# Optimization experiments

Hardware: AMD Instinct MI355X
Metric: run time of the kernel (lower is better)

The kernel has to match this reference:

```python
import jax, jax.numpy as jnp
import numpy as np
import math

NEG_BIG = -1e9

def setup_inputs() -> dict:
    key = jax.random.key(0)
    k1, k2, k3 = jax.random.split(key, 3)
    N, C, T = 16, 64, 2048
    qkv = jax.random.normal(k1, (N, 3 * C, T), dtype=jnp.float32)
    pos = jax.random.normal(k2, (N, C, T), dtype=jnp.float32)
    attn_mask = jax.random.randint(k3, (N, T, T), 0, 2) == 1  # bool mask, True = masked
    return {"qkv": qkv, "pos": pos, "attn_mask": attn_mask}

def reference(qkv, pos, attn_mask):
    ch = qkv.shape[1] // 3
    q, k, v = jnp.split(qkv, 3, axis=1)  # each [N, C, T]
    q = q + pos
    k = k + pos
    v = v + pos
    scale = 1.0 / math.sqrt(math.sqrt(ch))
    # [N, T, T] attention logits
    weight = jnp.einsum('bct,bcs->bts', q * scale, k * scale)
    weight = jnp.where(attn_mask, NEG_BIG, weight)
    weight = jax.nn.softmax(weight.astype(jnp.float32), axis=-1).astype(weight.dtype)
    return jnp.einsum('bts,bcs->bct', weight, v)
```

## Files before the change

kernel.cpp:

```cpp
#include <hip/hip_runtime.h>
#include <hip/hip_bf16.h>

typedef float f32x4 __attribute__((ext_vector_type(4)));
typedef short s16x8 __attribute__((ext_vector_type(8)));

#define L2E 1.44269504088896340736f

static __device__ __forceinline__ unsigned int bf16_rne(float f) {
    unsigned int u = __builtin_bit_cast(unsigned int, f);
    return (u + 0x7fffu + ((u >> 16) & 1u)) >> 16;
}
static __device__ __forceinline__ unsigned int pack_bf16x2(float lo, float hi) {
    return bf16_rne(lo) | (bf16_rne(hi) << 16);
}

__global__ __launch_bounds__(256) void qkv_prep(const float* __restrict__ qkv,
                                                const float* __restrict__ pos,
                                                unsigned short* __restrict__ qs,
                                                unsigned short* __restrict__ kt,
                                                unsigned short* __restrict__ vt)
{
    __shared__ unsigned short QtS[64][72];
    __shared__ unsigned short KtS[64][72];
    const int b    = blockIdx.y;
    const int t0   = blockIdx.x * 64;
    const int i    = threadIdx.x;
    const int crow = i >> 2;
    const int t16  = (i & 3) * 16;

    float pr[16];
    {
        const float* pp = pos + ((size_t)(b * 64 + crow)) * 2048 + t0 + t16;
        #pragma unroll
        for (int j = 0; j < 4; ++j) {
            float4 v = reinterpret_cast<const float4*>(pp)[j];
            pr[4*j+0] = v.x; pr[4*j+1] = v.y; pr[4*j+2] = v.z; pr[4*j+3] = v.w;
        }
    }
    const float* qp = qkv + ((size_t)(b * 192 + crow)) * 2048 + t0 + t16;
    {
        #pragma unroll
        for (int j = 0; j < 4; ++j) {
            float4 v = reinterpret_cast<const float4*>(qp)[j];
            QtS[t16 + 4*j + 0][crow] = (unsigned short)bf16_rne((v.x + pr[4*j+0]) * 0.125f);
            QtS[t16 + 4*j + 1][crow] = (unsigned short)bf16_rne((v.y + pr[4*j+1]) * 0.125f);
            QtS[t16 + 4*j + 2][crow] = (unsigned short)bf16_rne((v.z + pr[4*j+2]) * 0.125f);
            QtS[t16 + 4*j + 3][crow] = (unsigned short)bf16_rne((v.w + pr[4*j+3]) * 0.125f);
        }
    }
    {
        const float* kp = qp + (size_t)64 * 2048;
        #pragma unroll
        for (int j = 0; j < 4; ++j) {
            float4 v = reinterpret_cast<const float4*>(kp)[j];
            KtS[t16 + 4*j + 0][crow] = (unsigned short)bf16_rne(v.x + pr[4*j+0]);
            KtS[t16 + 4*j + 1][crow] = (unsigned short)bf16_rne(v.y + pr[4*j+1]);
            KtS[t16 + 4*j + 2][crow] = (unsigned short)bf16_rne(v.z + pr[4*j+2]);
            KtS[t16 + 4*j + 3][crow] = (unsigned short)bf16_rne(v.w + pr[4*j+3]);
        }
    }
    {
        const float* vp = qp + (size_t)128 * 2048;
        unsigned int vv[8];
        #pragma unroll
        for (int j = 0; j < 4; ++j) {
            float4 v = reinterpret_cast<const float4*>(vp)[j];
            vv[2*j+0] = pack_bf16x2(v.x + pr[4*j+0], v.y + pr[4*j+1]);
            vv[2*j+1] = pack_bf16x2(v.z + pr[4*j+2], v.w + pr[4*j+3]);
        }
        unsigned short* dst = vt + ((size_t)(b * 64 + crow)) * 2048 + t0 + t16;
        reinterpret_cast<uint4*>(dst)[0] = make_uint4(vv[0], vv[1], vv[2], vv[3]);
        reinterpret_cast<uint4*>(dst)[1] = make_uint4(vv[4], vv[5], vv[6], vv[7]);
    }
    __syncthreads();
    {
        const int trow = i >> 2;
        const int c16  = (i & 3) * 16;
        uint4 a0 = *reinterpret_cast<const uint4*>(&QtS[trow][c16]);
        uint4 a1 = *reinterpret_cast<const uint4*>(&QtS[trow][c16 + 8]);
        unsigned short* qd = qs + ((size_t)(b * 2048 + t0 + trow)) * 64 + c16;
        reinterpret_cast<uint4*>(qd)[0] = a0;
        reinterpret_cast<uint4*>(qd)[1] = a1;
        uint4 b0 = *reinterpret_cast<const uint4*>(&KtS[trow][c16]);
        uint4 b1 = *reinterpret_cast<const uint4*>(&KtS[trow][c16 + 8]);
        unsigned short* kd = kt + ((size_t)(b * 2048 + t0 + trow)) * 64 + c16;
        reinterpret_cast<uint4*>(kd)[0] = b0;
        reinterpret_cast<uint4*>(kd)[1] = b1;
    }
}

__global__ __launch_bounds__(256) void attn_kernel(const unsigned short* __restrict__ qs,
                                                   const unsigned short* __restrict__ kt,
                                                   const unsigned short* __restrict__ vt,
                                                   const void* __restrict__ maskp,
                                                   float* __restrict__ out)
{
    __shared__ unsigned short Klds[64][72];
    __shared__ unsigned short Vlds[64][72];
    __shared__ unsigned char  Mlds[64][80];

    const int b    = blockIdx.y;
    const int t0   = blockIdx.x * 64;
    const int tid  = threadIdx.x;
    const int wave = tid >> 6;
    const int lane = tid & 63;
    const int ln   = lane & 15;
    const int lg   = lane >> 4;

    unsigned int accm = 0;
    {
        const unsigned int* mu = (const unsigned int*)maskp;
        #pragma unroll
        for (int j = 0; j < 16; ++j) accm |= mu[j];
    }
    const bool maskIsBool = (accm & 0xffffff00u) != 0u;

    const int tg = t0 + 16 * wave + ln;
    s16x8 qf[2];
    #pragma unroll
    for (int kc = 0; kc < 2; ++kc)
        qf[kc] = *reinterpret_cast<const s16x8*>(
            qs + ((size_t)(b * 2048 + tg)) * 64 + 32 * kc + 8 * lg);

    f32x4 acc[4];
    #pragma unroll
    for (int n = 0; n < 4; ++n) acc[n] = (f32x4){0.f, 0.f, 0.f, 0.f};
    float M = -3.0e38f, L = 0.0f;

    const int stRow = tid >> 2;
    const int stC16 = (tid & 3) * 16;

    for (int st = 0; st < 32; ++st) {
        const int s0 = st * 64;
        {
            const unsigned short* src = kt + ((size_t)(b * 2048 + s0 + stRow)) * 64 + stC16;
            uint4 a0 = reinterpret_cast<const uint4*>(src)[0];
            uint4 a1 = reinterpret_cast<const uint4*>(src)[1];
            *reinterpret_cast<uint4*>(&Klds[stRow][stC16])     = a0;
            *reinterpret_cast<uint4*>(&Klds[stRow][stC16 + 8]) = a1;
        }
        {
            const unsigned short* src = vt + ((size_t)(b * 64 + stRow)) * 2048 + s0 + stC16;
            uint4 a0 = reinterpret_cast<const uint4*>(src)[0];
            uint4 a1 = reinterpret_cast<const uint4*>(src)[1];
            *reinterpret_cast<uint4*>(&Vlds[stRow][stC16])     = a0;
            *reinterpret_cast<uint4*>(&Vlds[stRow][stC16 + 8]) = a1;
        }
        if (maskIsBool) {
            const unsigned char* src = (const unsigned char*)maskp +
                ((size_t)b * 2048 + (size_t)(t0 + stRow)) * 2048 + s0 + stC16;
            *reinterpret_cast<uint4*>(&Mlds[stRow][stC16]) =
                *reinterpret_cast<const uint4*>(src);
        } else {
            const unsigned int* src = (const unsigned int*)maskp +
                ((size_t)b * 2048 + (size_t)(t0 + stRow)) * 2048 + s0 + stC16;
            uint4 x0 = reinterpret_cast<const uint4*>(src)[0];
            uint4 x1 = reinterpret_cast<const uint4*>(src)[1];
            uint4 x2 = reinterpret_cast<const uint4*>(src)[2];
            uint4 x3 = reinterpret_cast<const uint4*>(src)[3];
            auto p4 = [](uint4 x) {
                return (x.x ? 1u : 0u) | ((x.y ? 1u : 0u) << 8) |
                       ((x.z ? 1u : 0u) << 16) | ((x.w ? 1u : 0u) << 24);
            };
            *reinterpret_cast<uint4*>(&Mlds[stRow][stC16]) =
                make_uint4(p4(x0), p4(x1), p4(x2), p4(x3));
        }
        __syncthreads();

        f32x4 S[4];
        #pragma unroll
        for (int ti = 0; ti < 4; ++ti) S[ti] = (f32x4){0.f, 0.f, 0.f, 0.f};
        #pragma unroll
        for (int kc = 0; kc < 2; ++kc) {
            #pragma unroll
            for (int ti = 0; ti < 4; ++ti) {
                s16x8 kf = *reinterpret_cast<const s16x8*>(
                    &Klds[16 * ti + ln][32 * kc + 8 * lg]);
                S[ti] = __builtin_amdgcn_mfma_f32_16x16x32_bf16(kf, qf[kc], S[ti], 0, 0, 0);
            }
        }

        float p[4][4];
        const int mrow = 16 * wave + ln;
        #pragma unroll
        for (int ti = 0; ti < 4; ++ti) {
            unsigned int m32 = *reinterpret_cast<const unsigned int*>(
                &Mlds[mrow][16 * ti + 4 * lg]);
            #pragma unroll
            for (int r = 0; r < 4; ++r)
                p[ti][r] = ((m32 >> (8 * r)) & 0xffu) ? -1e9f : S[ti][r];
        }
        float tm = -3.0e38f;
        #pragma unroll
        for (int ti = 0; ti < 4; ++ti)
            #pragma unroll
            for (int r = 0; r < 4; ++r) tm = fmaxf(tm, p[ti][r]);
        tm = fmaxf(tm, __shfl_xor(tm, 16, 64));
        tm = fmaxf(tm, __shfl_xor(tm, 32, 64));
        const float Mn    = fmaxf(M, tm);
        const float alpha = exp2f((M - Mn) * L2E);
        float tsum = 0.f;
        #pragma unroll
        for (int ti = 0; ti < 4; ++ti)
            #pragma unroll
            for (int r = 0; r < 4; ++r) {
                p[ti][r] = exp2f((p[ti][r] - Mn) * L2E);
                tsum += p[ti][r];
            }
        tsum += __shfl_xor(tsum, 16, 64);
        tsum += __shfl_xor(tsum, 32, 64);
        L = L * alpha + tsum;
        M = Mn;
        #pragma unroll
        for (int n = 0; n < 4; ++n) acc[n] *= alpha;

        unsigned int pk[4][2];
        #pragma unroll
        for (int ti = 0; ti < 4; ++ti) {
            pk[ti][0] = pack_bf16x2(p[ti][0], p[ti][1]);
            pk[ti][1] = pack_bf16x2(p[ti][2], p[ti][3]);
        }
        unsigned int pf[2][4];
        #pragma unroll
        for (int kc2 = 0; kc2 < 2; ++kc2)
            #pragma unroll
            for (int a2 = 0; a2 < 2; ++a2)
                #pragma unroll
                for (int b2 = 0; b2 < 2; ++b2)
                    #pragma unroll
                    for (int e = 0; e < 2; ++e) {
                        int src = ln + 16 * (2 * (lg & 1) + e);
                        unsigned int v = (unsigned int)__shfl(
                            (int)pk[2 * kc2 + a2][b2], src, 64);
                        if ((lg >> 1) == a2) pf[kc2][2 * e + b2] = v;
                    }

        #pragma unroll
        for (int kc2 = 0; kc2 < 2; ++kc2) {
            union { unsigned int u[4]; s16x8 s; } pu;
            pu.u[0] = pf[kc2][0]; pu.u[1] = pf[kc2][1];
            pu.u[2] = pf[kc2][2]; pu.u[3] = pf[kc2][3];
            #pragma unroll
            for (int n = 0; n < 4; ++n) {
                s16x8 vf = *reinterpret_cast<const s16x8*>(
                    &Vlds[16 * n + ln][32 * kc2 + 8 * lg]);
                acc[n] = __builtin_amdgcn_mfma_f32_16x16x32_bf16(vf, pu.s, acc[n], 0, 0, 0);
            }
        }
        __syncthreads();
    }

    const float inv = 1.0f / L;
    #pragma unroll
    for (int n = 0; n < 4; ++n)
        #pragma unroll
        for (int r = 0; r < 4; ++r)
            out[((size_t)(b * 64 + 16 * n + 4 * lg + r)) * 2048 + t0 + 16 * wave + ln] =
                acc[n][r] * inv;
}

extern "C" void kernel_launch(void* const* d_in, const int* in_sizes, int n_in,
                              void* d_out, int out_size, void* d_ws, size_t ws_size,
                              hipStream_t stream) {
    const float* qkv = (const float*)d_in[0];
    const float* pos = (const float*)d_in[1];
    const void*  msk = d_in[2];
    float* outp = (float*)d_out;
    unsigned short* ws = (unsigned short*)d_ws;
    const size_t PLANE = (size_t)16 * 2048 * 64;
    unsigned short* qs = ws;
    unsigned short* kt = ws + PLANE;
    unsigned short* vt = ws + 2 * PLANE;

    dim3 grid(2048 / 64, 16);
    qkv_prep<<<grid, 256, 0, stream>>>(qkv, pos, qs, kt, vt);
    attn_kernel<<<grid, 256, 0, stream>>>(qs, kt, vt, msk, outp);
}
```

Before: 113.3 us.

## Double-buffer K/V in LDS, prefetch mask to registers, fold log2e into Q scale

```diff
diff --git a/kernel.cpp b/kernel.cpp
--- a/kernel.cpp
+++ b/kernel.cpp
@@ -2,6 +2,7 @@
 #include <hip/hip_bf16.h>
 
 typedef float f32x4 __attribute__((ext_vector_type(4)));
+typedef unsigned int u32x4 __attribute__((ext_vector_type(4)));
 typedef short s16x8 __attribute__((ext_vector_type(8)));
 
 #define L2E 1.44269504088896340736f
@@ -12,6 +13,11 @@
 }
 static __device__ __forceinline__ unsigned int pack_bf16x2(float lo, float hi) {
     return bf16_rne(lo) | (bf16_rne(hi) << 16);
+}
+static __device__ __forceinline__ unsigned int cvt_pk_bf16(float lo, float hi) {
+    unsigned int r;
+    asm("v_cvt_pk_bf16_f32 %0, %1, %2" : "=v"(r) : "v"(lo), "v"(hi));
+    return r;
 }
 
 __global__ __launch_bounds__(256) void qkv_prep(const float* __restrict__ qkv,
@@ -27,36 +33,38 @@
     const int i    = threadIdx.x;
     const int crow = i >> 2;
     const int t16  = (i & 3) * 16;
+    const float QSCALE = 0.125f * L2E;
 
     float pr[16];
     {
-        const float* pp = pos + ((size_t)(b * 64 + crow)) * 2048 + t0 + t16;
+        const f32x4* pp = reinterpret_cast<const f32x4*>(
+            pos + ((size_t)(b * 64 + crow)) * 2048 + t0 + t16);
         #pragma unroll
         for (int j = 0; j < 4; ++j) {
-            float4 v = reinterpret_cast<const float4*>(pp)[j];
-            pr[4*j+0] = v.x; pr[4*j+1] = v.y; pr[4*j+2] = v.z; pr[4*j+3] = v.w;
+            f32x4 v = __builtin_nontemporal_load(pp + j);
+            pr[4*j+0] = v[0]; pr[4*j+1] = v[1]; pr[4*j+2] = v[2]; pr[4*j+3] = v[3];
         }
     }
     const float* qp = qkv + ((size_t)(b * 192 + crow)) * 2048 + t0 + t16;
     {
         #pragma unroll
         for (int j = 0; j < 4; ++j) {
-            float4 v = reinterpret_cast<const float4*>(qp)[j];
-            QtS[t16 + 4*j + 0][crow] = (unsigned short)bf16_rne((v.x + pr[4*j+0]) * 0.125f);
-            QtS[t16 + 4*j + 1][crow] = (unsigned short)bf16_rne((v.y + pr[4*j+1]) * 0.125f);
-            QtS[t16 + 4*j + 2][crow] = (unsigned short)bf16_rne((v.z + pr[4*j+2]) * 0.125f);
-            QtS[t16 + 4*j + 3][crow] = (unsigned short)bf16_rne((v.w + pr[4*j+3]) * 0.125f);
+            f32x4 v = __builtin_nontemporal_load(reinterpret_cast<const f32x4*>(qp) + j);
+            #pragma unroll
+            for (int e = 0; e < 4; ++e)
+                QtS[t16 + 4*j + e][crow] =
+                    (unsigned short)bf16_rne((v[e] + pr[4*j+e]) * QSCALE);
         }
     }
     {
         const float* kp = qp + (size_t)64 * 2048;
         #pragma unroll
         for (int j = 0; j < 4; ++j) {
-            float4 v = reinterpret_cast<const float4*>(kp)[j];
-            KtS[t16 + 4*j + 0][crow] = (unsigned short)bf16_rne(v.x + pr[4*j+0]);
-            KtS[t16 + 4*j + 1][crow] = (unsigned short)bf16_rne(v.y + pr[4*j+1]);
-            KtS[t16 + 4*j + 2][crow] = (unsigned short)bf16_rne(v.z + pr[4*j+2]);
-            KtS[t16 + 4*j + 3][crow] = (unsigned short)bf16_rne(v.w + pr[4*j+3]);
+            f32x4 v = __builtin_nontemporal_load(reinterpret_cast<const f32x4*>(kp) + j);
+            #pragma unroll
+            for (int e = 0; e < 4; ++e)
+                KtS[t16 + 4*j + e][crow] =
+                    (unsigned short)bf16_rne(v[e] + pr[4*j+e]);
         }
     }
     {
@@ -64,28 +72,28 @@
         unsigned int vv[8];
         #pragma unroll
         for (int j = 0; j < 4; ++j) {
-            float4 v = reinterpret_cast<const float4*>(vp)[j];
-            vv[2*j+0] = pack_bf16x2(v.x + pr[4*j+0], v.y + pr[4*j+1]);
-            vv[2*j+1] = pack_bf16x2(v.z + pr[4*j+2], v.w + pr[4*j+3]);
+            f32x4 v = __builtin_nontemporal_load(reinterpret_cast<const f32x4*>(vp) + j);
+            vv[2*j+0] = pack_bf16x2(v[0] + pr[4*j+0], v[1] + pr[4*j+1]);
+            vv[2*j+1] = pack_bf16x2(v[2] + pr[4*j+2], v[3] + pr[4*j+3]);
         }
         unsigned short* dst = vt + ((size_t)(b * 64 + crow)) * 2048 + t0 + t16;
-        reinterpret_cast<uint4*>(dst)[0] = make_uint4(vv[0], vv[1], vv[2], vv[3]);
-        reinterpret_cast<uint4*>(dst)[1] = make_uint4(vv[4], vv[5], vv[6], vv[7]);
+        reinterpret_cast<u32x4*>(dst)[0] = (u32x4){vv[0], vv[1], vv[2], vv[3]};
+        reinterpret_cast<u32x4*>(dst)[1] = (u32x4){vv[4], vv[5], vv[6], vv[7]};
     }
     __syncthreads();
     {
         const int trow = i >> 2;
         const int c16  = (i & 3) * 16;
-        uint4 a0 = *reinterpret_cast<const uint4*>(&QtS[trow][c16]);
-        uint4 a1 = *reinterpret_cast<const uint4*>(&QtS[trow][c16 + 8]);
+        u32x4 a0 = *reinterpret_cast<const u32x4*>(&QtS[trow][c16]);
+        u32x4 a1 = *reinterpret_cast<const u32x4*>(&QtS[trow][c16 + 8]);
         unsigned short* qd = qs + ((size_t)(b * 2048 + t0 + trow)) * 64 + c16;
-        reinterpret_cast<uint4*>(qd)[0] = a0;
-        reinterpret_cast<uint4*>(qd)[1] = a1;
-        uint4 b0 = *reinterpret_cast<const uint4*>(&KtS[trow][c16]);
-        uint4 b1 = *reinterpret_cast<const uint4*>(&KtS[trow][c16 + 8]);
+        reinterpret_cast<u32x4*>(qd)[0] = a0;
+        reinterpret_cast<u32x4*>(qd)[1] = a1;
+        u32x4 b0 = *reinterpret_cast<const u32x4*>(&KtS[trow][c16]);
+        u32x4 b1 = *reinterpret_cast<const u32x4*>(&KtS[trow][c16 + 8]);
         unsigned short* kd = kt + ((size_t)(b * 2048 + t0 + trow)) * 64 + c16;
-        reinterpret_cast<uint4*>(kd)[0] = b0;
-        reinterpret_cast<uint4*>(kd)[1] = b1;
+        reinterpret_cast<u32x4*>(kd)[0] = b0;
+        reinterpret_cast<u32x4*>(kd)[1] = b1;
     }
 }
 
@@ -95,9 +103,8 @@
                                                    const void* __restrict__ maskp,
                                                    float* __restrict__ out)
 {
-    __shared__ unsigned short Klds[64][72];
-    __shared__ unsigned short Vlds[64][72];
-    __shared__ unsigned char  Mlds[64][80];
+    __shared__ unsigned short Klds[2][64][72];
+    __shared__ unsigned short Vlds[2][64][72];
 
     const int b    = blockIdx.y;
     const int t0   = blockIdx.x * 64;
@@ -129,98 +136,126 @@
 
     const int stRow = tid >> 2;
     const int stC16 = (tid & 3) * 16;
-
+    const unsigned short* kbase = kt + ((size_t)(b * 2048 + stRow)) * 64 + stC16;
+    const unsigned short* vbase = vt + ((size_t)(b * 64 + stRow)) * 2048 + stC16;
+    const size_t mrowoff = ((size_t)b * 2048 + (size_t)tg) * 2048;
+
+    unsigned int m_cur[4];
+
+    {
+        u32x4 ka0 = reinterpret_cast<const u32x4*>(kbase)[0];
+        u32x4 ka1 = reinterpret_cast<const u32x4*>(kbase)[1];
+        u32x4 va0 = reinterpret_cast<const u32x4*>(vbase)[0];
+        u32x4 va1 = reinterpret_cast<const u32x4*>(vbase)[1];
+        if (maskIsBool) {
+            const unsigned char* mp = (const unsigned char*)maskp + mrowoff + 4 * lg;
+            #pragma unroll
+            for (int ti = 0; ti < 4; ++ti)
+                m_cur[ti] = __builtin_nontemporal_load(
+                    reinterpret_cast<const unsigned int*>(mp + 16 * ti));
+        } else {
+            const u32x4* mp = reinterpret_cast<const u32x4*>(
+                (const unsigned int*)maskp + mrowoff + 4 * lg);
+            #pragma unroll
+            for (int ti = 0; ti < 4; ++ti) {
+                u32x4 x = __builtin_nontemporal_load(mp + 4 * ti);
+                m_cur[ti] = (x[0] ? 1u : 0u) | ((x[1] ? 1u : 0u) << 8) |
+                            ((x[2] ? 1u : 0u) << 16) | ((x[3] ? 1u : 0u) << 24);
+            }
+        }
+        *reinterpret_cast<u32x4*>(&Klds[0][stRow][stC16])     = ka0;
+        *reinterpret_cast<u32x4*>(&Klds[0][stRow][stC16 + 8]) = ka1;
+        *reinterpret_cast<u32x4*>(&Vlds[0][stRow][stC16])     = va0;
+        *reinterpret_cast<u32x4*>(&Vlds[0][stRow][stC16 + 8]) = va1;
+    }
+    __syncthreads();
+
+    int cur = 0;
     for (int st = 0; st < 32; ++st) {
-        const int s0 = st * 64;
-        {
-            const unsigned short* src = kt + ((size_t)(b * 2048 + s0 + stRow)) * 64 + stC16;
-            uint4 a0 = reinterpret_cast<const uint4*>(src)[0];
-            uint4 a1 = reinterpret_cast<const uint4*>(src)[1];
-            *reinterpret_cast<uint4*>(&Klds[stRow][stC16])     = a0;
-            *reinterpret_cast<uint4*>(&Klds[stRow][stC16 + 8]) = a1;
-        }
-        {
-            const unsigned short* src = vt + ((size_t)(b * 64 + stRow)) * 2048 + s0 + stC16;
-            uint4 a0 = reinterpret_cast<const uint4*>(src)[0];
-            uint4 a1 = reinterpret_cast<const uint4*>(src)[1];
-            *reinterpret_cast<uint4*>(&Vlds[stRow][stC16])     = a0;
-            *reinterpret_cast<uint4*>(&Vlds[stRow][stC16 + 8]) = a1;
-        }
-        if (maskIsBool) {
-            const unsigned char* src = (const unsigned char*)maskp +
-                ((size_t)b * 2048 + (size_t)(t0 + stRow)) * 2048 + s0 + stC16;
-            *reinterpret_cast<uint4*>(&Mlds[stRow][stC16]) =
-                *reinterpret_cast<const uint4*>(src);
-        } else {
-            const unsigned int* src = (const unsigned int*)maskp +
-                ((size_t)b * 2048 + (size_t)(t0 + stRow)) * 2048 + s0 + stC16;
-            uint4 x0 = reinterpret_cast<const uint4*>(src)[0];
-            uint4 x1 = reinterpret_cast<const uint4*>(src)[1];
-            uint4 x2 = reinterpret_cast<const uint4*>(src)[2];
-            uint4 x3 = reinterpret_cast<const uint4*>(src)[3];
-            auto p4 = [](uint4 x) {
-                return (x.x ? 1u : 0u) | ((x.y ? 1u : 0u) << 8) |
-                       ((x.z ? 1u : 0u) << 16) | ((x.w ? 1u : 0u) << 24);
-            };
-            *reinterpret_cast<uint4*>(&Mlds[stRow][stC16]) =
-                make_uint4(p4(x0), p4(x1), p4(x2), p4(x3));
-        }
-        __syncthreads();
+        u32x4 ka0, ka1, va0, va1;
+        unsigned int m_nxt[4];
+        const bool pf = (st < 31);
+        if (pf) {
+            const int s1 = (st + 1) * 64;
+            const unsigned short* ks = kbase + (size_t)s1 * 64;
+            const unsigned short* vs = vbase + s1;
+            ka0 = reinterpret_cast<const u32x4*>(ks)[0];
+            ka1 = reinterpret_cast<const u32x4*>(ks)[1];
+            va0 = reinterpret_cast<const u32x4*>(vs)[0];
+            va1 = reinterpret_cast<const u32x4*>(vs)[1];
+            if (maskIsBool) {
+                const unsigned char* mp = (const unsigned char*)maskp + mrowoff + s1 + 4 * lg;
+                #pragma unroll
+                for (int ti = 0; ti < 4; ++ti)
+                    m_nxt[ti] = __builtin_nontemporal_load(
+                        reinterpret_cast<const unsigned int*>(mp + 16 * ti));
+            } else {
+                const u32x4* mp = reinterpret_cast<const u32x4*>(
+                    (const unsigned int*)maskp + mrowoff + s1 + 4 * lg);
+                #pragma unroll
+                for (int ti = 0; ti < 4; ++ti) {
+                    u32x4 x = __builtin_nontemporal_load(mp + 4 * ti);
+                    m_nxt[ti] = (x[0] ? 1u : 0u) | ((x[1] ? 1u : 0u) << 8) |
+                                ((x[2] ? 1u : 0u) << 16) | ((x[3] ? 1u : 0u) << 24);
+                }
+            }
+        }
 
         f32x4 S[4];
         #pragma unroll
         for (int ti = 0; ti < 4; ++ti) S[ti] = (f32x4){0.f, 0.f, 0.f, 0.f};
+        __builtin_amdgcn_s_setprio(1);
         #pragma unroll
         for (int kc = 0; kc < 2; ++kc) {
             #pragma unroll
             for (int ti = 0; ti < 4; ++ti) {
                 s16x8 kf = *reinterpret_cast<const s16x8*>(
-                    &Klds[16 * ti + ln][32 * kc + 8 * lg]);
+                    &Klds[cur][16 * ti + ln][32 * kc + 8 * lg]);
                 S[ti] = __builtin_amdgcn_mfma_f32_16x16x32_bf16(kf, qf[kc], S[ti], 0, 0, 0);
             }
         }
+        __builtin_amdgcn_s_setprio(0);
 
         float p[4][4];
-        const int mrow = 16 * wave + ln;
         #pragma unroll
         for (int ti = 0; ti < 4; ++ti) {
-            unsigned int m32 = *reinterpret_cast<const unsigned int*>(
-                &Mlds[mrow][16 * ti + 4 * lg]);
             #pragma unroll
             for (int r = 0; r < 4; ++r)
-                p[ti][r] = ((m32 >> (8 * r)) & 0xffu) ? -1e9f : S[ti][r];
-        }
-        float tm = -3.0e38f;
-        #pragma unroll
-        for (int ti = 0; ti < 4; ++ti)
-            #pragma unroll
-            for (int r = 0; r < 4; ++r) tm = fmaxf(tm, p[ti][r]);
+                p[ti][r] = ((m_cur[ti] >> (8 * r)) & 0xffu) ? -1e9f : S[ti][r];
+        }
+        float tm = fmaxf(fmaxf(fmaxf(p[0][0], p[0][1]), fmaxf(p[0][2], p[0][3])),
+                         fmaxf(fmaxf(p[1][0], p[1][1]), fmaxf(p[1][2], p[1][3])));
+        tm = fmaxf(tm, fmaxf(fmaxf(fmaxf(p[2][0], p[2][1]), fmaxf(p[2][2], p[2][3])),
+                             fmaxf(fmaxf(p[3][0], p[3][1]), fmaxf(p[3][2], p[3][3]))));
         tm = fmaxf(tm, __shfl_xor(tm, 16, 64));
         tm = fmaxf(tm, __shfl_xor(tm, 32, 64));
-        const float Mn    = fmaxf(M, tm);
-        const float alpha = exp2f((M - Mn) * L2E);
+        if (!__all(tm <= M)) {
+            const float Mn    = fmaxf(M, tm);
+            const float alpha = exp2f(M - Mn);
+            L *= alpha;
+            #pragma unroll
+            for (int n = 0; n < 4; ++n) acc[n] *= alpha;
+            M = Mn;
+        }
         float tsum = 0.f;
         #pragma unroll
         for (int ti = 0; ti < 4; ++ti)
             #pragma unroll
             for (int r = 0; r < 4; ++r) {
-                p[ti][r] = exp2f((p[ti][r] - Mn) * L2E);
+                p[ti][r] = exp2f(p[ti][r] - M);
                 tsum += p[ti][r];
             }
         tsum += __shfl_xor(tsum, 16, 64);
         tsum += __shfl_xor(tsum, 32, 64);
-        L = L * alpha + tsum;
-        M = Mn;
-        #pragma unroll
-        for (int n = 0; n < 4; ++n) acc[n] *= alpha;
+        L += tsum;
 
         unsigned int pk[4][2];
         #pragma unroll
         for (int ti = 0; ti < 4; ++ti) {
-            pk[ti][0] = pack_bf16x2(p[ti][0], p[ti][1]);
-            pk[ti][1] = pack_bf16x2(p[ti][2], p[ti][3]);
-        }
-        unsigned int pf[2][4];
+            pk[ti][0] = cvt_pk_bf16(p[ti][0], p[ti][1]);
+            pk[ti][1] = cvt_pk_bf16(p[ti][2], p[ti][3]);
+        }
+        unsigned int pfr[2][4];
         #pragma unroll
         for (int kc2 = 0; kc2 < 2; ++kc2)
             #pragma unroll
@@ -232,22 +267,34 @@
                         int src = ln + 16 * (2 * (lg & 1) + e);
                         unsigned int v = (unsigned int)__shfl(
                             (int)pk[2 * kc2 + a2][b2], src, 64);
-                        if ((lg >> 1) == a2) pf[kc2][2 * e + b2] = v;
+                        if ((lg >> 1) == a2) pfr[kc2][2 * e + b2] = v;
                     }
 
+        __builtin_amdgcn_s_setprio(1);
         #pragma unroll
         for (int kc2 = 0; kc2 < 2; ++kc2) {
             union { unsigned int u[4]; s16x8 s; } pu;
-            pu.u[0] = pf[kc2][0]; pu.u[1] = pf[kc2][1];
-            pu.u[2] = pf[kc2][2]; pu.u[3] = pf[kc2][3];
+            pu.u[0] = pfr[kc2][0]; pu.u[1] = pfr[kc2][1];
+            pu.u[2] = pfr[kc2][2]; pu.u[3] = pfr[kc2][3];
             #pragma unroll
             for (int n = 0; n < 4; ++n) {
                 s16x8 vf = *reinterpret_cast<const s16x8*>(
-                    &Vlds[16 * n + ln][32 * kc2 + 8 * lg]);
+                    &Vlds[cur][16 * n + ln][32 * kc2 + 8 * lg]);
                 acc[n] = __builtin_amdgcn_mfma_f32_16x16x32_bf16(vf, pu.s, acc[n], 0, 0, 0);
             }
         }
-        __syncthreads();
+        __builtin_amdgcn_s_setprio(0);
+
+        if (pf) {
+            *reinterpret_cast<u32x4*>(&Klds[cur ^ 1][stRow][stC16])     = ka0;
+            *reinterpret_cast<u32x4*>(&Klds[cur ^ 1][stRow][stC16 + 8]) = ka1;
+            *reinterpret_cast<u32x4*>(&Vlds[cur ^ 1][stRow][stC16])     = va0;
+            *reinterpret_cast<u32x4*>(&Vlds[cur ^ 1][stRow][stC16 + 8]) = va1;
+            #pragma unroll
+            for (int ti = 0; ti < 4; ++ti) m_cur[ti] = m_nxt[ti];
+            __syncthreads();
+            cur ^= 1;
+        }
     }
 
     const float inv = 1.0f / L;
@@ -255,8 +302,9 @@
     for (int n = 0; n < 4; ++n)
         #pragma unroll
         for (int r = 0; r < 4; ++r)
-            out[((size_t)(b * 64 + 16 * n + 4 * lg + r)) * 2048 + t0 + 16 * wave + ln] =
-                acc[n][r] * inv;
+            __builtin_nontemporal_store(
+                acc[n][r] * inv,
+                &out[((size_t)(b * 64 + 16 * n + 4 * lg + r)) * 2048 + t0 + 16 * wave + ln]);
 }
 
 extern "C" void kernel_launch(void* const* d_in, const int* in_sizes, int n_in,
```

Result: no change. 114.0 us (+0.6%).
